# Performance work log

Measured on AMD Instinct MI355X. Metric: run time of the kernel, lower is better.

## Reference

```python
import jax, jax.numpy as jnp
import numpy as np

B, H, K, E = 8, 256, 256, 128
VOCAB, FVOCAB = 30000, 1000


def setup_inputs() -> dict:
    key = jax.random.key(0)
    k1, k2, k3, k4, k5, k6 = jax.random.split(key, 6)
    key_emb = jax.random.normal(k2, (VOCAB, E), dtype=jnp.float32)
    value_emb = jax.random.normal(k3, (FVOCAB, E), dtype=jnp.float32)
    # padding_idx=0 rows are zero
    key_emb = key_emb.at[0].set(0.0)
    value_emb = value_emb.at[0].set(0.0)
    return {
        "hidden": jax.random.normal(k1, (B, H, E), dtype=jnp.float32),
        "key_emb": key_emb,
        "value_emb": value_emb,
        "key_seq": jax.random.randint(k4, (B, K), 0, VOCAB, dtype=jnp.int64) if jax.config.jax_enable_x64 else jax.random.randint(k4, (B, K), 0, VOCAB).astype(jnp.int32),
        "value_seq": jax.random.randint(k5, (B, H, K), 0, FVOCAB).astype(jnp.int32),
        "mask_matrix": jax.random.randint(k6, (B, H, K), 0, 2).astype(jnp.int32),
    }


def reference(hidden, key_emb, value_emb, key_seq, value_seq, mask_matrix):
    scale = jnp.asarray(np.power(E, 0.5), dtype=jnp.float32)
    # embedding gathers (padding_idx=0 -> zero row, enforced in setup)
    k = key_emb[key_seq]            # [B, K, E]
    v = value_emb[value_seq]        # [B, H, K, E]
    # masked exp-normalize attention (manual, not softmax: no max-subtract)
    u = jnp.einsum('bhe,bke->bhk', hidden, k) / scale   # [B, H, K]
    delta = jnp.exp(u) * mask_matrix.astype(jnp.float32)
    p = delta / (jnp.sum(delta, axis=2, keepdims=True) + 1e-10)  # [B, H, K]
    # attention-weighted value aggregation
    o = jnp.einsum('bhk,bhke->bhe', p, v)               # [B, H, E]
    # nonzero-count averaging over H
    aspect_len = jnp.sum(o != 0, axis=1).astype(jnp.float32)     # [B, E]
    avg_o = jnp.sum(o, axis=1) / aspect_len                      # [B, E]
    return avg_o
```

## Files before the change

### kernel.cpp

```cpp
#include <hip/hip_runtime.h>
#include <math.h>

#define BB 8
#define HH 256
#define KK 256
#define EE 128

template <int CTRL, int RM>
__device__ __forceinline__ float dpp_add(float x) {
    int d = __builtin_amdgcn_update_dpp(0, __float_as_int(x), CTRL, RM, 0xf, true);
    return x + __int_as_float(d);
}
__device__ __forceinline__ float dpp_reduce_half(float x) {
    x = dpp_add<0x111, 0xf>(x);
    x = dpp_add<0x112, 0xf>(x);
    x = dpp_add<0x114, 0xf>(x);
    x = dpp_add<0x118, 0xf>(x);
    x = dpp_add<0x142, 0xa>(x);
    return x;
}
__device__ __forceinline__ float dpp_reduce_wave(float x) {
    x = dpp_reduce_half(x);
    x = dpp_add<0x143, 0xc>(x);
    return x;
}

__global__ __launch_bounds__(256) void kvmn_bh(
    const float* __restrict__ hidden,
    const float* __restrict__ key_emb,
    const float* __restrict__ value_emb,
    const int*   __restrict__ key_seq,
    const int*   __restrict__ value_seq,
    const int*   __restrict__ mask,
    float* __restrict__ o_ws)
{
    __shared__ float  sh_u[KK];
    __shared__ float  sh_part[4];
    __shared__ float4 sh_o4[8][32];

    const int bid  = blockIdx.x;
    const int b    = bid >> 8;
    const int h    = bid & 255;
    const int tid  = threadIdx.x;
    const int w    = tid >> 6;
    const int lane = tid & 63;
    const int half = lane >> 5;
    const int sub  = lane & 31;

    const int ksreg = key_seq[b * KK + tid];
    const int vsreg = value_seq[(size_t)(b * HH + h) * KK + tid];
    const int my_mask = mask[(size_t)(b * HH + h) * KK + tid];

    const float4 h4 = *(const float4*)&hidden[(size_t)(b * HH + h) * EE + sub * 4];

    const float inv_scale = 0.08838834764831845f;

    #pragma unroll 16
    for (int i = 0; i < 32; ++i) {
        const int    row = __shfl(ksreg, half * 32 + i, 64);
        const float4 kv  = *(const float4*)&key_emb[(size_t)row * EE + sub * 4];
        float part = kv.x * h4.x + kv.y * h4.y + kv.z * h4.z + kv.w * h4.w;
        part = dpp_reduce_half(part);
        if (sub == 31) sh_u[w * 64 + half * 32 + i] = part * inv_scale;
    }
    __syncthreads();

    const float d = expf(sh_u[tid]) * (float)my_mask;
    float s = dpp_reduce_wave(d);
    if (lane == 63) sh_part[w] = s;
    __syncthreads();
    const float denom = sh_part[0] + sh_part[1] + sh_part[2] + sh_part[3];
    const float pk = d * (1.0f / (denom + 1e-10f));

    float4 acc = make_float4(0.f, 0.f, 0.f, 0.f);
    #pragma unroll 16
    for (int i = 0; i < 32; ++i) {
        const int    src = half * 32 + i;
        const float  p   = __shfl(pk, src, 64);
        const int    row = __shfl(vsreg, src, 64);
        const float4 v   = *(const float4*)&value_emb[(size_t)row * EE + sub * 4];
        acc.x += p * v.x;
        acc.y += p * v.y;
        acc.z += p * v.z;
        acc.w += p * v.w;
    }
    sh_o4[w * 2 + half][sub] = acc;
    __syncthreads();

    if (tid < 32) {
        float4 t = sh_o4[0][tid];
        #pragma unroll
        for (int r = 1; r < 8; ++r) {
            const float4 q = sh_o4[r][tid];
            t.x += q.x; t.y += q.y; t.z += q.z; t.w += q.w;
        }
        *(float4*)&o_ws[(size_t)(b * HH + h) * EE + tid * 4] = t;
    }
}

__global__ __launch_bounds__(256) void kvmn_reduce(
    const float* __restrict__ o_ws,
    float* __restrict__ out)
{
    __shared__ float sh_sum[256];
    __shared__ int   sh_cnt[256];

    const int b  = blockIdx.x;
    const int t  = threadIdx.x;
    const int e  = t & 127;
    const int hh = t >> 7;

    float sum = 0.0f;
    int   cnt = 0;
    const float* base = o_ws + (size_t)(b * HH + hh * 128) * EE + e;
    #pragma unroll 8
    for (int h = 0; h < 128; ++h) {
        const float v = base[(size_t)h * EE];
        sum += v;
        cnt += (v != 0.0f) ? 1 : 0;
    }
    sh_sum[t] = sum;
    sh_cnt[t] = cnt;
    __syncthreads();
    if (t < 128) {
        const float s = sh_sum[t] + sh_sum[t + 128];
        const int   c = sh_cnt[t] + sh_cnt[t + 128];
        out[b * EE + t] = s / (float)c;
    }
}

extern "C" void kernel_launch(void* const* d_in, const int* in_sizes, int n_in,
                              void* d_out, int out_size, void* d_ws, size_t ws_size,
                              hipStream_t stream) {
    const float* hidden    = (const float*)d_in[0];
    const float* key_emb   = (const float*)d_in[1];
    const float* value_emb = (const float*)d_in[2];
    const int*   key_seq   = (const int*)d_in[3];
    const int*   value_seq = (const int*)d_in[4];
    const int*   mask      = (const int*)d_in[5];

    float* o_ws = (float*)d_ws;

    kvmn_bh<<<BB * HH, 256, 0, stream>>>(hidden, key_emb, value_emb,
                                         key_seq, value_seq, mask, o_ws);
    kvmn_reduce<<<BB, 256, 0, stream>>>(o_ws, (float*)d_out);
    (void)in_sizes; (void)n_in; (void)out_size; (void)ws_size;
}
```

Before: 102.7 us.

## Split score computation into separate kernel reusing key gathers across four rows

Moves the hidden·key score computation out of the per-(b,h) attention kernel into its own kernel, where each block handles four h rows and reuses each gathered key embedding row for all four dot products. Scores are written to a workspace buffer and read back by the attention kernel, which now only does exp-normalize and value aggregation. This cuts redundant key gathers fourfold at the cost of an extra launch and a global round trip for the score matrix. It also precomputes the value row offset with a shift.

```diff
diff --git a/kernel.cpp b/kernel.cpp
--- a/kernel.cpp
+++ b/kernel.cpp
@@ -25,16 +25,60 @@
     return x;
 }
 
-__global__ __launch_bounds__(256) void kvmn_bh(
+__global__ __launch_bounds__(256) void kvmn_u(
     const float* __restrict__ hidden,
     const float* __restrict__ key_emb,
+    const int*   __restrict__ key_seq,
+    float* __restrict__ u_ws)
+{
+    const int bid  = blockIdx.x;
+    const int b    = bid >> 6;
+    const int h0   = (bid & 63) << 2;
+    const int tid  = threadIdx.x;
+    const int w    = tid >> 6;
+    const int lane = tid & 63;
+    const int half = lane >> 5;
+    const int sub  = lane & 31;
+
+    const int ksreg = key_seq[b * KK + tid];
+
+    const float4 hq0 = *(const float4*)&hidden[(size_t)(b * HH + h0 + 0) * EE + sub * 4];
+    const float4 hq1 = *(const float4*)&hidden[(size_t)(b * HH + h0 + 1) * EE + sub * 4];
+    const float4 hq2 = *(const float4*)&hidden[(size_t)(b * HH + h0 + 2) * EE + sub * 4];
+    const float4 hq3 = *(const float4*)&hidden[(size_t)(b * HH + h0 + 3) * EE + sub * 4];
+
+    const float inv_scale = 0.08838834764831845f;
+    float* ub = u_ws + (size_t)(b * HH + h0) * KK;
+
+    #pragma unroll 8
+    for (int i = 0; i < 32; ++i) {
+        const int    k   = w * 64 + half * 32 + i;
+        const int    row = __shfl(ksreg, half * 32 + i, 64);
+        const float4 kv  = *(const float4*)&key_emb[(size_t)row * EE + sub * 4];
+        float p0 = kv.x * hq0.x + kv.y * hq0.y + kv.z * hq0.z + kv.w * hq0.w;
+        float p1 = kv.x * hq1.x + kv.y * hq1.y + kv.z * hq1.z + kv.w * hq1.w;
+        float p2 = kv.x * hq2.x + kv.y * hq2.y + kv.z * hq2.z + kv.w * hq2.w;
+        float p3 = kv.x * hq3.x + kv.y * hq3.y + kv.z * hq3.z + kv.w * hq3.w;
+        p0 = dpp_reduce_half(p0) * inv_scale;
+        p1 = dpp_reduce_half(p1) * inv_scale;
+        p2 = dpp_reduce_half(p2) * inv_scale;
+        p3 = dpp_reduce_half(p3) * inv_scale;
+        if (sub == 31) {
+            ub[0 * KK + k] = p0;
+            ub[1 * KK + k] = p1;
+            ub[2 * KK + k] = p2;
+            ub[3 * KK + k] = p3;
+        }
+    }
+}
+
+__global__ __launch_bounds__(256) void kvmn_attn(
     const float* __restrict__ value_emb,
-    const int*   __restrict__ key_seq,
     const int*   __restrict__ value_seq,
     const int*   __restrict__ mask,
+    const float* __restrict__ u_ws,
     float* __restrict__ o_ws)
 {
-    __shared__ float  sh_u[KK];
     __shared__ float  sh_part[4];
     __shared__ float4 sh_o4[8][32];
 
@@ -47,25 +91,13 @@
     const int half = lane >> 5;
     const int sub  = lane & 31;
 
-    const int ksreg = key_seq[b * KK + tid];
-    const int vsreg = value_seq[(size_t)(b * HH + h) * KK + tid];
-    const int my_mask = mask[(size_t)(b * HH + h) * KK + tid];
+    const size_t bh = (size_t)(b * HH + h);
+    const int   vsreg   = value_seq[bh * KK + tid];
+    const int   voff    = vsreg << 7;
+    const int   my_mask = mask[bh * KK + tid];
+    const float u       = u_ws[bh * KK + tid];
 
-    const float4 h4 = *(const float4*)&hidden[(size_t)(b * HH + h) * EE + sub * 4];
-
-    const float inv_scale = 0.08838834764831845f;
-
-    #pragma unroll 16
-    for (int i = 0; i < 32; ++i) {
-        const int    row = __shfl(ksreg, half * 32 + i, 64);
-        const float4 kv  = *(const float4*)&key_emb[(size_t)row * EE + sub * 4];
-        float part = kv.x * h4.x + kv.y * h4.y + kv.z * h4.z + kv.w * h4.w;
-        part = dpp_reduce_half(part);
-        if (sub == 31) sh_u[w * 64 + half * 32 + i] = part * inv_scale;
-    }
-    __syncthreads();
-
-    const float d = expf(sh_u[tid]) * (float)my_mask;
+    const float d = expf(u) * (float)my_mask;
     float s = dpp_reduce_wave(d);
     if (lane == 63) sh_part[w] = s;
     __syncthreads();
@@ -77,8 +109,8 @@
     for (int i = 0; i < 32; ++i) {
         const int    src = half * 32 + i;
         const float  p   = __shfl(pk, src, 64);
-        const int    row = __shfl(vsreg, src, 64);
-        const float4 v   = *(const float4*)&value_emb[(size_t)row * EE + sub * 4];
+        const int    ro  = __shfl(voff, src, 64);
+        const float4 v   = *(const float4*)&value_emb[(size_t)ro + sub * 4];
         acc.x += p * v.x;
         acc.y += p * v.y;
         acc.z += p * v.z;
@@ -94,7 +126,7 @@
             const float4 q = sh_o4[r][tid];
             t.x += q.x; t.y += q.y; t.z += q.z; t.w += q.w;
         }
-        *(float4*)&o_ws[(size_t)(b * HH + h) * EE + tid * 4] = t;
+        *(float4*)&o_ws[bh * EE + tid * 4] = t;
     }
 }
 
@@ -140,9 +172,10 @@
     const int*   mask      = (const int*)d_in[5];
 
     float* o_ws = (float*)d_ws;
+    float* u_ws = (float*)d_ws + (size_t)BB * HH * EE;
 
-    kvmn_bh<<<BB * HH, 256, 0, stream>>>(hidden, key_emb, value_emb,
-                                         key_seq, value_seq, mask, o_ws);
+    kvmn_u<<<BB * 64, 256, 0, stream>>>(hidden, key_emb, key_seq, u_ws);
+    kvmn_attn<<<BB * HH, 256, 0, stream>>>(value_emb, value_seq, mask, u_ws, o_ws);
     kvmn_reduce<<<BB, 256, 0, stream>>>(o_ws, (float*)d_out);
     (void)in_sizes; (void)n_in; (void)out_size; (void)ws_size;
 }
```

New measurement: 105.8 us. 3.1% more time.

## Fuse H-reduction into main kernel via last-block atomic ticket

Applied to the files above, without the earlier changes.

Merges the separate reduce kernel into the per-(b,h) kernel. Each block bumps an atomic counter per batch after writing its output row, and the last block to finish a batch performs the sum and nonzero-count averaging over H. This removes one kernel launch and the gap between launches, but adds a memset launch, a fence and an atomic per block, and extra shared memory that could affect occupancy.

```diff
diff --git a/kernel.cpp b/kernel.cpp
--- a/kernel.cpp
+++ b/kernel.cpp
@@ -25,18 +25,23 @@
     return x;
 }
 
-__global__ __launch_bounds__(256) void kvmn_bh(
+__global__ __launch_bounds__(256) void kvmn_fused(
     const float* __restrict__ hidden,
     const float* __restrict__ key_emb,
     const float* __restrict__ value_emb,
     const int*   __restrict__ key_seq,
     const int*   __restrict__ value_seq,
     const int*   __restrict__ mask,
-    float* __restrict__ o_ws)
+    float* __restrict__ o_ws,
+    int*   __restrict__ done,
+    float* __restrict__ out)
 {
     __shared__ float  sh_u[KK];
     __shared__ float  sh_part[4];
     __shared__ float4 sh_o4[8][32];
+    __shared__ float  sh_sum[256];
+    __shared__ int    sh_cnt[256];
+    __shared__ int    sh_ticket;
 
     const int bid  = blockIdx.x;
     const int b    = bid >> 8;
@@ -96,36 +101,37 @@
         }
         *(float4*)&o_ws[(size_t)(b * HH + h) * EE + tid * 4] = t;
     }
-}
+    __syncthreads();
 
-__global__ __launch_bounds__(256) void kvmn_reduce(
-    const float* __restrict__ o_ws,
-    float* __restrict__ out)
-{
-    __shared__ float sh_sum[256];
-    __shared__ int   sh_cnt[256];
+    if (tid == 0) {
+        __threadfence();
+        sh_ticket = __hip_atomic_fetch_add(&done[b], 1, __ATOMIC_ACQ_REL,
+                                           __HIP_MEMORY_SCOPE_AGENT);
+    }
+    __syncthreads();
+    if (sh_ticket != HH - 1) return;
 
-    const int b  = blockIdx.x;
-    const int t  = threadIdx.x;
-    const int e  = t & 127;
-    const int hh = t >> 7;
-
-    float sum = 0.0f;
-    int   cnt = 0;
-    const float* base = o_ws + (size_t)(b * HH + hh * 128) * EE + e;
-    #pragma unroll 8
-    for (int h = 0; h < 128; ++h) {
-        const float v = base[(size_t)h * EE];
-        sum += v;
-        cnt += (v != 0.0f) ? 1 : 0;
-    }
-    sh_sum[t] = sum;
-    sh_cnt[t] = cnt;
-    __syncthreads();
-    if (t < 128) {
-        const float s = sh_sum[t] + sh_sum[t + 128];
-        const int   c = sh_cnt[t] + sh_cnt[t + 128];
-        out[b * EE + t] = s / (float)c;
+    __threadfence();
+    {
+        const int e  = tid & 127;
+        const int hh = tid >> 7;
+        float sum = 0.0f;
+        int   cnt = 0;
+        const float* base = o_ws + (size_t)(b * HH + hh * 128) * EE + e;
+        #pragma unroll 8
+        for (int hi = 0; hi < 128; ++hi) {
+            const float v = base[(size_t)hi * EE];
+            sum += v;
+            cnt += (v != 0.0f) ? 1 : 0;
+        }
+        sh_sum[tid] = sum;
+        sh_cnt[tid] = cnt;
+        __syncthreads();
+        if (tid < 128) {
+            const float fs = sh_sum[tid] + sh_sum[tid + 128];
+            const int   fc = sh_cnt[tid] + sh_cnt[tid + 128];
+            out[b * EE + tid] = fs / (float)fc;
+        }
     }
 }
 
@@ -140,9 +146,12 @@
     const int*   mask      = (const int*)d_in[5];
 
     float* o_ws = (float*)d_ws;
+    int*   done = (int*)((char*)d_ws + (size_t)BB * HH * EE * sizeof(float));
 
-    kvmn_bh<<<BB * HH, 256, 0, stream>>>(hidden, key_emb, value_emb,
-                                         key_seq, value_seq, mask, o_ws);
-    kvmn_reduce<<<BB, 256, 0, stream>>>(o_ws, (float*)d_out);
+    hipMemsetAsync(done, 0, BB * sizeof(int), stream);
+
+    kvmn_fused<<<BB * HH, 256, 0, stream>>>(hidden, key_emb, value_emb,
+                                            key_seq, value_seq, mask,
+                                            o_ws, done, (float*)d_out);
     (void)in_sizes; (void)n_in; (void)out_size; (void)ws_size;
 }
```

Result: slower. 193.3 us (+88.3%).

## Compute attention scores per-thread dot products and stage p/value offsets in LDS

Applied to the files above, without the earlier changes.

The score phase now has each thread compute a full dot product over its own key row, reading the hidden vector from shared memory. This replaces the half-wave cooperative loads and DPP reductions. Attention weights and prescaled value row offsets are staged in LDS as float2 and read with broadcast loads, replacing two cross-lane shuffles per iteration, and occupancy is hinted with launch_bounds(256,8). The trade-off is that per-thread key-row reads are uncoalesced, each thread strides across a whole row, and the change adds extra syncthreads.

```diff
diff --git a/kernel.cpp b/kernel.cpp
--- a/kernel.cpp
+++ b/kernel.cpp
@@ -25,7 +25,7 @@
     return x;
 }
 
-__global__ __launch_bounds__(256) void kvmn_bh(
+__global__ __launch_bounds__(256, 8) void kvmn_bh(
     const float* __restrict__ hidden,
     const float* __restrict__ key_emb,
     const float* __restrict__ value_emb,
@@ -34,8 +34,9 @@
     const int*   __restrict__ mask,
     float* __restrict__ o_ws)
 {
-    __shared__ float  sh_u[KK];
+    __shared__ float4 sh_h4[32];
     __shared__ float  sh_part[4];
+    __shared__ float2 sh_pv[KK];
     __shared__ float4 sh_o4[8][32];
 
     const int bid  = blockIdx.x;
@@ -47,38 +48,48 @@
     const int half = lane >> 5;
     const int sub  = lane & 31;
 
-    const int ksreg = key_seq[b * KK + tid];
-    const int vsreg = value_seq[(size_t)(b * HH + h) * KK + tid];
-    const int my_mask = mask[(size_t)(b * HH + h) * KK + tid];
+    const size_t bh = (size_t)(b * HH + h);
 
-    const float4 h4 = *(const float4*)&hidden[(size_t)(b * HH + h) * EE + sub * 4];
+    const int ksreg   = key_seq[b * KK + tid];
+    const int vsreg   = value_seq[bh * KK + tid];
+    const int my_mask = mask[bh * KK + tid];
+
+    if (tid < 32) sh_h4[tid] = *(const float4*)&hidden[bh * EE + tid * 4];
+    __syncthreads();
 
     const float inv_scale = 0.08838834764831845f;
 
-    #pragma unroll 16
+    const float* krow = &key_emb[(size_t)ksreg * EE];
+    float4 acc1 = make_float4(0.f, 0.f, 0.f, 0.f);
+    #pragma unroll 4
     for (int i = 0; i < 32; ++i) {
-        const int    row = __shfl(ksreg, half * 32 + i, 64);
-        const float4 kv  = *(const float4*)&key_emb[(size_t)row * EE + sub * 4];
-        float part = kv.x * h4.x + kv.y * h4.y + kv.z * h4.z + kv.w * h4.w;
-        part = dpp_reduce_half(part);
-        if (sub == 31) sh_u[w * 64 + half * 32 + i] = part * inv_scale;
+        const float4 kv = *(const float4*)&krow[i * 4];
+        const float4 hv = sh_h4[i];
+        acc1.x += kv.x * hv.x;
+        acc1.y += kv.y * hv.y;
+        acc1.z += kv.z * hv.z;
+        acc1.w += kv.w * hv.w;
     }
-    __syncthreads();
+    const float u = ((acc1.x + acc1.y) + (acc1.z + acc1.w)) * inv_scale;
 
-    const float d = expf(sh_u[tid]) * (float)my_mask;
+    const float d = expf(u) * (float)my_mask;
     float s = dpp_reduce_wave(d);
     if (lane == 63) sh_part[w] = s;
     __syncthreads();
     const float denom = sh_part[0] + sh_part[1] + sh_part[2] + sh_part[3];
     const float pk = d * (1.0f / (denom + 1e-10f));
 
+    sh_pv[tid] = make_float2(pk, __int_as_float(vsreg << 7));
+    __syncthreads();
+
     float4 acc = make_float4(0.f, 0.f, 0.f, 0.f);
-    #pragma unroll 16
+    const int kbase = w * 64 + half * 32;
+    #pragma unroll 8
     for (int i = 0; i < 32; ++i) {
-        const int    src = half * 32 + i;
-        const float  p   = __shfl(pk, src, 64);
-        const int    row = __shfl(vsreg, src, 64);
-        const float4 v   = *(const float4*)&value_emb[(size_t)row * EE + sub * 4];
+        const float2 pv = sh_pv[kbase + i];
+        const float  p  = pv.x;
+        const int    ro = __float_as_int(pv.y);
+        const float4 v  = *(const float4*)&value_emb[(size_t)ro + sub * 4];
         acc.x += p * v.x;
         acc.y += p * v.y;
         acc.z += p * v.z;
@@ -94,7 +105,7 @@
             const float4 q = sh_o4[r][tid];
             t.x += q.x; t.y += q.y; t.z += q.z; t.w += q.w;
         }
-        *(float4*)&o_ws[(size_t)(b * HH + h) * EE + tid * 4] = t;
+        *(float4*)&o_ws[bh * EE + tid * 4] = t;
     }
 }
 
```

Result: slower. 115.4 us (+12.4%).
